# Performance work log

Hardware: AMD Instinct MI355X
Metric: run time of the kernel (lower is better)

## Reference

```python
import jax, jax.numpy as jnp
import numpy as np

B, C, D, K = 65536, 128, 32, 10
EPS = 1e-12


def setup_inputs() -> dict:
    key = jax.random.key(0)
    k1, k2, k3, k4 = jax.random.split(key, 4)
    data = jax.random.normal(k1, (B, D), dtype=jnp.float32)
    mu = jax.random.normal(k2, (C, D), dtype=jnp.float32)
    # S_inv must be symmetric positive definite (inverse covariance per cluster)
    A = 0.1 * jax.random.normal(k3, (C, D, D), dtype=jnp.float32)
    S_inv = jnp.einsum('cij,ckj->cik', A, A) + jnp.eye(D, dtype=jnp.float32)[None]
    # one-hot class assignment per cluster (int32), as stored in the module
    cls = jax.random.randint(k4, (C,), 0, K)
    cluster_labels = jax.nn.one_hot(cls, K, dtype=jnp.int32)
    return {"data": data, "mu": mu, "S_inv": S_inv, "cluster_labels": cluster_labels}


def reference(data, mu, S_inv, cluster_labels):
    # Mahalanobis distance d2[b,c] = (z_b - mu_c)^T S_inv_c (z_b - mu_c),
    # expanded to avoid a [B, C, D] diff tensor.
    zz = data[:, :, None] * data[:, None, :]            # [B, D, D]
    t1 = jnp.einsum('bde,cde->bc', zz, S_inv)           # z' Sinv z
    Sm = jnp.einsum('cde,ce->cd', S_inv, mu)            # [C, D]
    t2 = data @ Sm.T                                    # z' Sinv mu  [B, C]
    t3 = jnp.einsum('cd,cd->c', mu, Sm)                 # mu' Sinv mu [C]
    d2 = t1 - 2.0 * t2 + t3[None, :]                    # [B, C]
    Gamma = jnp.exp(-0.5 * d2)                          # Gaussian activation
    # defuzzify_batch: normalize activations, project through one-hot labels
    norm_gamma = Gamma / (jnp.sum(Gamma, axis=1, keepdims=True) + EPS)
    label_scores = norm_gamma @ cluster_labels.astype(jnp.float32)  # [B, K]
    preds = jnp.argmax(label_scores, axis=1)
    clusters = jnp.argmax(Gamma, axis=1)
    return label_scores, preds, clusters
```

## Files before the change

### kernel.cpp

```cpp
#include <hip/hip_runtime.h>
#include <cmath>

#define B_N 65536
#define C_N 128
#define D_N 32
#define K_N 10
#define EPS_F 1e-12f
#define SCALE_F (-0.72134752044448169f)

#define NKK 48
#define QFRAG_N (4 * NKK * 64 * 8)
#define YSTR 41

typedef _Float16 f16x8 __attribute__((ext_vector_type(8)));
typedef float    f32x16 __attribute__((ext_vector_type(16)));

__device__ __forceinline__ void mdkk(int kk, int& dA, int& e0) {
    int w = (kk >= 17) + (kk >= 30) + (kk >= 39) + (kk >= 44);
    int off = w == 0 ? 0 : (w == 1 ? 17 : (w == 2 ? 30 : (w == 3 ? 39 : 44)));
    int r = kk - off;
    dA = 2 * r;
    e0 = 2 * r + 8 * w;
}

__global__ __launch_bounds__(128) void k_prep(const float* __restrict__ S,
                                              const float* __restrict__ mu,
                                              const int* __restrict__ onehot,
                                              _Float16* __restrict__ Qh,
                                              _Float16* __restrict__ Ql,
                                              int* __restrict__ cls) {
    const int c = blockIdx.x;
    const int tid = threadIdx.x;
    __shared__ float sSm[D_N];
    __shared__ float st3;

    if (tid < D_N) {
        const float* Sr = S + (size_t)c * (D_N * D_N) + (size_t)tid * D_N;
        const float* mr = mu + (size_t)c * D_N;
        float a0 = 0.f, a1 = 0.f;
#pragma unroll
        for (int e = 0; e < D_N; e += 2) {
            a0 = fmaf(Sr[e + 0], mr[e + 0], a0);
            a1 = fmaf(Sr[e + 1], mr[e + 1], a1);
        }
        sSm[tid] = a0 + a1;
    }
    __syncthreads();
    if (tid == 0) {
        const float* mr = mu + (size_t)c * D_N;
        float a = 0.f;
#pragma unroll
        for (int d = 0; d < D_N; ++d) a = fmaf(mr[d], sSm[d], a);
        st3 = a;
        int cl = 0;
#pragma unroll
        for (int k = 0; k < K_N; ++k)
            if (onehot[c * K_N + k] != 0) cl = k;
        cls[c] = cl;
    }
    __syncthreads();

    if (tid < 2 * NKK) {
        const int kk   = tid >> 1;
        const int half = tid & 1;
        int dA, e0;
        mdkk(kk, dA, e0);
        const int d  = dA + half;
        const int ct = c >> 5;
        const size_t base =
            ((size_t)(ct * NKK + kk) * 64 + half * 32 + (c & 31)) * 8;
        const float* Sc = S + (size_t)c * (D_N * D_N);
        for (int j = 0; j < 8; ++j) {
            const int e = e0 + j;
            float q = 0.f;
            if (d <= e && e <= 32) {
                float v;
                if (e < 32)      v = Sc[d * D_N + e] * (d == e ? 1.f : 2.f);
                else if (d < 32) v = -2.f * sSm[d];
                else             v = st3;
                q = SCALE_F * v;
            }
            _Float16 h = (_Float16)q;
            Qh[base + j] = h;
            Ql[base + j] = (_Float16)(q - (float)h);
        }
    }
}

__device__ __forceinline__ void ldq(const f16x8* __restrict__ QH,
                                    const f16x8* __restrict__ QL,
                                    int kk, int lane,
                                    f16x8 (&qh)[4], f16x8 (&ql)[4]) {
#pragma unroll
    for (int ct = 0; ct < 4; ++ct) {
        qh[ct] = QH[(ct * NKK + kk) * 64 + lane];
        ql[ct] = QL[(ct * NKK + kk) * 64 + lane];
    }
}

__device__ __forceinline__ void ldy(const float* sy, int ybase, int hioff,
                                    int kk, float& yd, float (&yw)[8]) {
    int dA, e0;
    mdkk(kk, dA, e0);
    yd = sy[ybase + dA + hioff];
#pragma unroll
    for (int j = 0; j < 8; ++j) yw[j] = sy[ybase + e0 + j];
}

__device__ __forceinline__ void domfma(const f16x8 (&qh)[4], const f16x8 (&ql)[4],
                                       float yd, const float (&yw)[8],
                                       f32x16 (&acc)[4]) {
    f16x8 ph, pl;
#pragma unroll
    for (int j = 0; j < 8; ++j) {
        float f = yd * yw[j];
        _Float16 h = (_Float16)f;
        ph[j] = h;
        pl[j] = (_Float16)(f - (float)h);
    }
#pragma unroll
    for (int ct = 0; ct < 4; ++ct)
        acc[ct] = __builtin_amdgcn_mfma_f32_32x32x16_f16(qh[ct], ph, acc[ct], 0, 0, 0);
#pragma unroll
    for (int ct = 0; ct < 4; ++ct)
        acc[ct] = __builtin_amdgcn_mfma_f32_32x32x16_f16(ql[ct], ph, acc[ct], 0, 0, 0);
#pragma unroll
    for (int ct = 0; ct < 4; ++ct)
        acc[ct] = __builtin_amdgcn_mfma_f32_32x32x16_f16(qh[ct], pl, acc[ct], 0, 0, 0);
}

__global__ __launch_bounds__(256, 2) void k_mainv5(const float* __restrict__ data,
                                                   const _Float16* __restrict__ Qhp,
                                                   const _Float16* __restrict__ Qlp,
                                                   const int* __restrict__ clsp,
                                                   float* __restrict__ out) {
    const int tid  = threadIdx.x;
    const int lane = tid & 63;
    const int wid  = tid >> 6;
    const int b0w  = blockIdx.x * 128 + wid * 32;
    const int col  = lane & 31;
    const bool hi  = lane >= 32;

    __shared__ float sy[256 * YSTR + 64];
    __shared__ int lcls[C_N];
    if (tid < C_N) lcls[tid] = clsp[tid];

    const int ybase = tid * YSTR;
    {
        const float4* p0 = (const float4*)(data + (size_t)(b0w + col) * D_N);
#pragma unroll
        for (int i = 0; i < 8; ++i) {
            float4 v = p0[i];
            sy[ybase + 4 * i + 0] = v.x;
            sy[ybase + 4 * i + 1] = v.y;
            sy[ybase + 4 * i + 2] = v.z;
            sy[ybase + 4 * i + 3] = v.w;
        }
        sy[ybase + 32] = 1.f;
#pragma unroll
        for (int i = 33; i < YSTR; ++i) sy[ybase + i] = 0.f;
        if (tid < 64) sy[256 * YSTR + tid] = 0.f;
    }
    __syncthreads();

    f32x16 acc[4];
#pragma unroll
    for (int ct = 0; ct < 4; ++ct)
#pragma unroll
        for (int g = 0; g < 16; ++g) acc[ct][g] = 0.f;

    const f16x8* QH = (const f16x8*)Qhp;
    const f16x8* QL = (const f16x8*)Qlp;
    const int hioff = hi ? 1 : 0;

    f16x8 qhA[4], qlA[4], qhB[4], qlB[4], qhC[4], qlC[4];
    float ydA, ywA[8], ydB, ywB[8], ydC, ywC[8];

    ldq(QH, QL, 0, lane, qhA, qlA);
    ldq(QH, QL, 1, lane, qhB, qlB);
    ldq(QH, QL, 2, lane, qhC, qlC);
    ldy(sy, ybase, hioff, 0, ydA, ywA);

#pragma clang loop unroll(disable)
    for (int kk = 0; kk < NKK; kk += 3) {
        ldy(sy, ybase, hioff, kk + 1, ydB, ywB);
        domfma(qhA, qlA, ydA, ywA, acc);
        { int t = kk + 3 < NKK ? kk + 3 : NKK - 1;
          ldq(QH, QL, t, lane, qhA, qlA); }
        ldy(sy, ybase, hioff, kk + 2, ydC, ywC);
        domfma(qhB, qlB, ydB, ywB, acc);
        { int t = kk + 4 < NKK ? kk + 4 : NKK - 1;
          ldq(QH, QL, t, lane, qhB, qlB); }
        { int t = kk + 3 < NKK ? kk + 3 : NKK - 1;
          ldy(sy, ybase, hioff, t, ydA, ywA); }
        domfma(qhC, qlC, ydC, ywC, acc);
        { int t = kk + 5 < NKK ? kk + 5 : NKK - 1;
          ldq(QH, QL, t, lane, qhC, qlC); }
    }

    const float hoff = hi ? 4.f : 0.f;
    const int* lc = lcls + (hi ? 4 : 0);
    float sum = 0.f, gmax = -1.f, gcf = 0.f;
    float a0 = 0, a1 = 0, a2 = 0, a3 = 0, a4 = 0, a5 = 0, a6 = 0, a7 = 0, a8 = 0, a9 = 0;
#pragma unroll
    for (int ct = 0; ct < 4; ++ct) {
        float psum = 0.f;
#pragma unroll
        for (int g = 0; g < 16; ++g) {
            float v = acc[ct][g];
            float gm;
            asm("v_exp_f32 %0, %1" : "=v"(gm) : "v"(v));
            const int cbase = ct * 32 + (g & 3) + 8 * (g >> 2);
            int cl = lc[cbase];
            psum += gm;
            float cf = (float)cbase + hoff;
            if (gm > gmax) { gmax = gm; gcf = cf; }
            a0 += (cl == 0) ? gm : 0.f;
            a1 += (cl == 1) ? gm : 0.f;
            a2 += (cl == 2) ? gm : 0.f;
            a3 += (cl == 3) ? gm : 0.f;
            a4 += (cl == 4) ? gm : 0.f;
            a5 += (cl == 5) ? gm : 0.f;
            a6 += (cl == 6) ? gm : 0.f;
            a7 += (cl == 7) ? gm : 0.f;
            a8 += (cl == 8) ? gm : 0.f;
            a9 += (cl == 9) ? gm : 0.f;
        }
        sum += psum;
    }

    sum += __shfl_xor(sum, 32, 64);
    {
        float om = __shfl_xor(gmax, 32, 64);
        float oc = __shfl_xor(gcf, 32, 64);
        bool take = (om > gmax) || (om == gmax && oc < gcf);
        if (take) { gmax = om; gcf = oc; }
    }
    a0 += __shfl_xor(a0, 32, 64);
    a1 += __shfl_xor(a1, 32, 64);
    a2 += __shfl_xor(a2, 32, 64);
    a3 += __shfl_xor(a3, 32, 64);
    a4 += __shfl_xor(a4, 32, 64);
    a5 += __shfl_xor(a5, 32, 64);
    a6 += __shfl_xor(a6, 32, 64);
    a7 += __shfl_xor(a7, 32, 64);
    a8 += __shfl_xor(a8, 32, 64);
    a9 += __shfl_xor(a9, 32, 64);

    if (!hi) {
        const int b = b0w + col;
        float inv = 1.0f / (sum + EPS_F);
        float ls[K_N] = {a0 * inv, a1 * inv, a2 * inv, a3 * inv, a4 * inv,
                         a5 * inv, a6 * inv, a7 * inv, a8 * inv, a9 * inv};
        float best = -1.f;
        int bk = 0;
#pragma unroll
        for (int k = 0; k < K_N; ++k)
            if (ls[k] > best) { best = ls[k]; bk = k; }
        float2* o2 = (float2*)(out + (size_t)b * K_N);
#pragma unroll
        for (int k2 = 0; k2 < K_N / 2; ++k2)
            o2[k2] = make_float2(ls[2 * k2], ls[2 * k2 + 1]);
        out[(size_t)B_N * K_N + b] = (float)bk;
        out[(size_t)B_N * K_N + B_N + b] = gcf;
    }
}

extern "C" void kernel_launch(void* const* d_in, const int* in_sizes, int n_in,
                              void* d_out, int out_size, void* d_ws, size_t ws_size,
                              hipStream_t stream) {
    const float* data   = (const float*)d_in[0];
    const float* mu     = (const float*)d_in[1];
    const float* S      = (const float*)d_in[2];
    const int*   onehot = (const int*)d_in[3];
    float* out = (float*)d_out;

    _Float16* Qh  = (_Float16*)d_ws;
    _Float16* Ql  = Qh + QFRAG_N;
    int*      cls = (int*)(Ql + QFRAG_N);

    hipLaunchKernelGGL(k_prep, dim3(C_N), dim3(128), 0, stream,
                       S, mu, onehot, Qh, Ql, cls);
    hipLaunchKernelGGL(k_mainv5, dim3(B_N / 128), dim3(256), 0, stream,
                       data, Qh, Ql, cls, out);
}
```

Before: 114.3 us.

## Stage Q fragments through double-buffered LDS with direct global-to-LDS loads

Interleaves the hi and lo Q fragments into per-step 4096-half chunks. Each block now stages a chunk cooperatively into a double-buffered LDS area using global_load_lds, instead of every wave loading all fragments from global memory into registers. This removes redundant global traffic and register pressure, at the cost of two block barriers per step pair and about 16 KB more shared memory. It also trims the padded step count from 48 to 46 and splits products into hi/lo halves with packed round-toward-zero converts, which changes rounding slightly.

Result: faster. 106.6 us (-6.7%).

```diff
diff --git a/kernel.cpp b/kernel.cpp
--- a/kernel.cpp
+++ b/kernel.cpp
@@ -8,14 +8,16 @@
 #define EPS_F 1e-12f
 #define SCALE_F (-0.72134752044448169f)
 
-#define NKK 48
-#define QFRAG_N (4 * NKK * 64 * 8)
+#define NKK 46
+#define CHUNK_F16 4096
+#define QF_N (NKK * CHUNK_F16)
 #define YSTR 41
 
 typedef _Float16 f16x8 __attribute__((ext_vector_type(8)));
 typedef float    f32x16 __attribute__((ext_vector_type(16)));
 
 __device__ __forceinline__ void mdkk(int kk, int& dA, int& e0) {
+    if (kk >= 45) { dA = 0; e0 = 0; return; }
     int w = (kk >= 17) + (kk >= 30) + (kk >= 39) + (kk >= 44);
     int off = w == 0 ? 0 : (w == 1 ? 17 : (w == 2 ? 30 : (w == 3 ? 39 : 44)));
     int r = kk - off;
@@ -26,8 +28,7 @@
 __global__ __launch_bounds__(128) void k_prep(const float* __restrict__ S,
                                               const float* __restrict__ mu,
                                               const int* __restrict__ onehot,
-                                              _Float16* __restrict__ Qh,
-                                              _Float16* __restrict__ Ql,
+                                              _Float16* __restrict__ QF,
                                               int* __restrict__ cls) {
     const int c = blockIdx.x;
     const int tid = threadIdx.x;
@@ -67,13 +68,13 @@
         mdkk(kk, dA, e0);
         const int d  = dA + half;
         const int ct = c >> 5;
-        const size_t base =
-            ((size_t)(ct * NKK + kk) * 64 + half * 32 + (c & 31)) * 8;
+        const size_t base = (size_t)kk * CHUNK_F16 + ct * 1024
+                          + (size_t)(half * 32 + (c & 31)) * 8;
         const float* Sc = S + (size_t)c * (D_N * D_N);
         for (int j = 0; j < 8; ++j) {
             const int e = e0 + j;
             float q = 0.f;
-            if (d <= e && e <= 32) {
+            if (kk < 45 && d <= e && e <= 32) {
                 float v;
                 if (e < 32)      v = Sc[d * D_N + e] * (d == e ? 1.f : 2.f);
                 else if (d < 32) v = -2.f * sSm[d];
@@ -81,20 +82,26 @@
                 q = SCALE_F * v;
             }
             _Float16 h = (_Float16)q;
-            Qh[base + j] = h;
-            Ql[base + j] = (_Float16)(q - (float)h);
-        }
-    }
-}
-
-__device__ __forceinline__ void ldq(const f16x8* __restrict__ QH,
-                                    const f16x8* __restrict__ QL,
-                                    int kk, int lane,
-                                    f16x8 (&qh)[4], f16x8 (&ql)[4]) {
-#pragma unroll
-    for (int ct = 0; ct < 4; ++ct) {
-        qh[ct] = QH[(ct * NKK + kk) * 64 + lane];
-        ql[ct] = QL[(ct * NKK + kk) * 64 + lane];
+            QF[base + j]       = h;
+            QF[base + 512 + j] = (_Float16)(q - (float)h);
+        }
+    }
+}
+
+__device__ __forceinline__ void gl_lds16(const void* g, void* l) {
+    __builtin_amdgcn_global_load_lds(
+        (const __attribute__((address_space(1))) unsigned int*)g,
+        (__attribute__((address_space(3))) unsigned int*)l, 16, 0, 0);
+}
+
+__device__ __forceinline__ void stage_chunk(const _Float16* __restrict__ QF,
+                                            _Float16* __restrict__ dst,
+                                            int chunk, int wid, int lane) {
+#pragma unroll
+    for (int i = 0; i < 2; ++i) {
+        const int slot = i * 4 + wid;
+        gl_lds16(QF + (size_t)chunk * CHUNK_F16 + slot * 512 + lane * 8,
+                 dst + slot * 512);
     }
 }
 
@@ -107,16 +114,26 @@
     for (int j = 0; j < 8; ++j) yw[j] = sy[ybase + e0 + j];
 }
 
-__device__ __forceinline__ void domfma(const f16x8 (&qh)[4], const f16x8 (&ql)[4],
-                                       float yd, const float (&yw)[8],
-                                       f32x16 (&acc)[4]) {
+__device__ __forceinline__ void step_compute(const _Float16* __restrict__ buf,
+                                             int lane, float yd, const float (&yw)[8],
+                                             f32x16 (&acc)[4]) {
+    const f16x8* qb = (const f16x8*)buf;
+    f16x8 qh[4], ql[4];
+#pragma unroll
+    for (int ct = 0; ct < 4; ++ct) {
+        qh[ct] = qb[ct * 128 + lane];
+        ql[ct] = qb[ct * 128 + 64 + lane];
+    }
     f16x8 ph, pl;
 #pragma unroll
-    for (int j = 0; j < 8; ++j) {
-        float f = yd * yw[j];
-        _Float16 h = (_Float16)f;
-        ph[j] = h;
-        pl[j] = (_Float16)(f - (float)h);
+    for (int j = 0; j < 8; j += 2) {
+        float f0 = yd * yw[j], f1 = yd * yw[j + 1];
+        auto h2 = __builtin_amdgcn_cvt_pkrtz(f0, f1);
+        float r0 = f0 - (float)h2[0];
+        float r1 = f1 - (float)h2[1];
+        auto l2 = __builtin_amdgcn_cvt_pkrtz(r0, r1);
+        ph[j] = h2[0]; ph[j + 1] = h2[1];
+        pl[j] = l2[0]; pl[j + 1] = l2[1];
     }
 #pragma unroll
     for (int ct = 0; ct < 4; ++ct)
@@ -129,9 +146,8 @@
         acc[ct] = __builtin_amdgcn_mfma_f32_32x32x16_f16(qh[ct], pl, acc[ct], 0, 0, 0);
 }
 
-__global__ __launch_bounds__(256, 2) void k_mainv5(const float* __restrict__ data,
-                                                   const _Float16* __restrict__ Qhp,
-                                                   const _Float16* __restrict__ Qlp,
+__global__ __launch_bounds__(256, 2) void k_mainv6(const float* __restrict__ data,
+                                                   const _Float16* __restrict__ QF,
                                                    const int* __restrict__ clsp,
                                                    float* __restrict__ out) {
     const int tid  = threadIdx.x;
@@ -142,6 +158,7 @@
     const bool hi  = lane >= 32;
 
     __shared__ float sy[256 * YSTR + 64];
+    __shared__ alignas(16) _Float16 qbuf[2][CHUNK_F16];
     __shared__ int lcls[C_N];
     if (tid < C_N) lcls[tid] = clsp[tid];
 
@@ -161,41 +178,31 @@
         for (int i = 33; i < YSTR; ++i) sy[ybase + i] = 0.f;
         if (tid < 64) sy[256 * YSTR + tid] = 0.f;
     }
+
+    f32x16 acc[4];
+#pragma unroll
+    for (int ct = 0; ct < 4; ++ct)
+#pragma unroll
+        for (int g = 0; g < 16; ++g) acc[ct][g] = 0.f;
+
+    stage_chunk(QF, &qbuf[0][0], 0, wid, lane);
+    stage_chunk(QF, &qbuf[1][0], 1, wid, lane);
     __syncthreads();
 
-    f32x16 acc[4];
-#pragma unroll
-    for (int ct = 0; ct < 4; ++ct)
-#pragma unroll
-        for (int g = 0; g < 16; ++g) acc[ct][g] = 0.f;
-
-    const f16x8* QH = (const f16x8*)Qhp;
-    const f16x8* QL = (const f16x8*)Qlp;
     const int hioff = hi ? 1 : 0;
-
-    f16x8 qhA[4], qlA[4], qhB[4], qlB[4], qhC[4], qlC[4];
-    float ydA, ywA[8], ydB, ywB[8], ydC, ywC[8];
-
-    ldq(QH, QL, 0, lane, qhA, qlA);
-    ldq(QH, QL, 1, lane, qhB, qlB);
-    ldq(QH, QL, 2, lane, qhC, qlC);
+    float ydA, ywA[8], ydB, ywB[8];
     ldy(sy, ybase, hioff, 0, ydA, ywA);
 
 #pragma clang loop unroll(disable)
-    for (int kk = 0; kk < NKK; kk += 3) {
-        ldy(sy, ybase, hioff, kk + 1, ydB, ywB);
-        domfma(qhA, qlA, ydA, ywA, acc);
-        { int t = kk + 3 < NKK ? kk + 3 : NKK - 1;
-          ldq(QH, QL, t, lane, qhA, qlA); }
-        ldy(sy, ybase, hioff, kk + 2, ydC, ywC);
-        domfma(qhB, qlB, ydB, ywB, acc);
-        { int t = kk + 4 < NKK ? kk + 4 : NKK - 1;
-          ldq(QH, QL, t, lane, qhB, qlB); }
-        { int t = kk + 3 < NKK ? kk + 3 : NKK - 1;
-          ldy(sy, ybase, hioff, t, ydA, ywA); }
-        domfma(qhC, qlC, ydC, ywC, acc);
-        { int t = kk + 5 < NKK ? kk + 5 : NKK - 1;
-          ldq(QH, QL, t, lane, qhC, qlC); }
+    for (int t = 0; t < NKK; t += 2) {
+        ldy(sy, ybase, hioff, t + 1, ydB, ywB);
+        step_compute(&qbuf[0][0], lane, ydA, ywA, acc);
+        __syncthreads();
+        if (t + 2 < NKK) stage_chunk(QF, &qbuf[0][0], t + 2, wid, lane);
+        ldy(sy, ybase, hioff, t + 2, ydA, ywA);
+        step_compute(&qbuf[1][0], lane, ydB, ywB, acc);
+        __syncthreads();
+        if (t + 3 < NKK) stage_chunk(QF, &qbuf[1][0], t + 3, wid, lane);
     }
 
     const float hoff = hi ? 4.f : 0.f;
@@ -275,12 +282,11 @@
     const int*   onehot = (const int*)d_in[3];
     float* out = (float*)d_out;
 
-    _Float16* Qh  = (_Float16*)d_ws;
-    _Float16* Ql  = Qh + QFRAG_N;
-    int*      cls = (int*)(Ql + QFRAG_N);
+    _Float16* QF  = (_Float16*)d_ws;
+    int*      cls = (int*)(QF + QF_N);
 
     hipLaunchKernelGGL(k_prep, dim3(C_N), dim3(128), 0, stream,
-                       S, mu, onehot, Qh, Ql, cls);
-    hipLaunchKernelGGL(k_mainv5, dim3(B_N / 128), dim3(256), 0, stream,
-                       data, Qh, Ql, cls, out);
-}
+                       S, mu, onehot, QF, cls);
+    hipLaunchKernelGGL(k_mainv6, dim3(B_N / 128), dim3(256), 0, stream,
+                       data, QF, cls, out);
+}
```
